# Kernel optimization log

Hardware: AMD Instinct MI355X
Metric: run time of the kernel (lower is better)

The kernel has to match this reference:

```python
import jax, jax.numpy as jnp
import numpy as np

B, C, H, W = 16, 256, 64, 64
D = C // 8  # query/key bottleneck dim


def setup_inputs() -> dict:
    key = jax.random.key(0)
    k1, k2, k3, k4 = jax.random.split(key, 4)
    x = jax.random.normal(k1, (B, C, H, W), dtype=jnp.float32)
    # 1x1 Conv1d weights (spectral-norm applied weights treated as given params)
    Wq = jax.random.normal(k2, (D, C), dtype=jnp.float32) * (1.0 / np.sqrt(C))
    Wk = jax.random.normal(k3, (D, C), dtype=jnp.float32) * (1.0 / np.sqrt(C))
    Wv = jax.random.normal(k4, (C, C), dtype=jnp.float32) * (1.0 / np.sqrt(C))
    gamma = jnp.array(0.5, dtype=jnp.float32)  # nonzero so attention path is exercised
    return {"x": x, "Wq": Wq, "Wk": Wk, "Wv": Wv, "gamma": gamma}


def reference(x, Wq, Wk, Wv, gamma):
    Bb, Cc, Hh, Ww = x.shape
    N = Hh * Ww
    flat = x.reshape(Bb, Cc, N)                    # [B, C, N]
    q = jnp.einsum('dc,bcn->bnd', Wq, flat)        # [B, N, D]
    k = jnp.einsum('dc,bcn->bdn', Wk, flat)        # [B, D, N]
    v = jnp.einsum('ec,bcn->ben', Wv, flat)        # [B, C, N]
    qk = jnp.einsum('bnd,bdm->bnm', q, k)          # [B, N, N]
    attn = jax.nn.softmax(qk, axis=1)              # NOTE: softmax over dim=1 (query axis), as in source
    out = jnp.einsum('ben,bnm->bem', v, attn)      # [B, C, N]
    out = out.reshape(Bb, Cc, Hh, Ww)
    return gamma * out + x
```

## Files before the change

### kernel.cpp

```cpp
#include <hip/hip_runtime.h>
#include <math.h>
#include <stdint.h>

#define NB 16
#define NC 256
#define NN 4096
#define ND 32

typedef __bf16 bf16_t;
typedef __bf16 bf16x4 __attribute__((ext_vector_type(4)));
typedef __bf16 bf16x8 __attribute__((ext_vector_type(8)));
typedef float  f32x4  __attribute__((ext_vector_type(4)));

#define AS_GLOBAL __attribute__((address_space(1)))
#define AS_LDS    __attribute__((address_space(3)))

__global__ __launch_bounds__(256) void wconv(
    const float* __restrict__ Wq, const float* __restrict__ Wk,
    const float* __restrict__ Wv, bf16_t* __restrict__ Wb, bf16_t* __restrict__ Wlo)
{
    int i = blockIdx.x * 256 + threadIdx.x;
    if (i >= 320 * 256) return;
    int row = i >> 8, c = i & 255;
    float v;
    if (row < 256)      v = Wv[(row      ) * 256 + c];
    else if (row < 288) v = Wq[(row - 256) * 256 + c] * 1.44269504088896340736f;
    else                v = Wk[(row - 288) * 256 + c];
    bf16_t h = (bf16_t)v;
    Wb[i] = h;
    if (row >= 256) Wlo[(row - 256) * 256 + c] = (bf16_t)(v - (float)h);
}

#define BN_P  128
#define KSTEP 64
#define XPAD  130

__global__ __launch_bounds__(512) void proj_mfma(
    const float* __restrict__ x, const bf16_t* __restrict__ Wb,
    const bf16_t* __restrict__ Wlo,
    bf16_t* __restrict__ Pqb, bf16_t* __restrict__ Pkb, bf16_t* __restrict__ Vn)
{
    __shared__ float xt[KSTEP][XPAD];

    const int b  = blockIdx.x >> 5;
    const int n0 = (blockIdx.x & 31) * BN_P;
    const int tid  = threadIdx.x;
    const int lane = tid & 63;
    const int w    = tid >> 6;
    const int mstrip = w >> 1;
    const int nh     = w & 1;
    const int llo = lane & 15, lhi = lane >> 4;
    const bool qkwave = (mstrip == 3);

    const float* xb = x + (size_t)b * NC * NN + n0;

    f32x4 acc[5][4];
    #pragma unroll
    for (int mf = 0; mf < 5; ++mf)
        #pragma unroll
        for (int nf = 0; nf < 4; ++nf)
            acc[mf][nf] = (f32x4){0.f,0.f,0.f,0.f};

    for (int k0 = 0; k0 < NC; k0 += KSTEP) {
        #pragma unroll
        for (int p = 0; p < 4; ++p) {
            int idx = p * 512 + tid;
            int c   = idx >> 5;
            int nn  = (idx & 31) << 2;
            float4 v = *(const float4*)(xb + (size_t)(k0 + c) * NN + nn);
            *(float2*)&xt[c][nn]     = make_float2(v.x, v.y);
            *(float2*)&xt[c][nn + 2] = make_float2(v.z, v.w);
        }
        __syncthreads();

        #pragma unroll
        for (int ks = 0; ks < 2; ++ks) {
            bf16x8 Ah[5], Al[4];
            #pragma unroll
            for (int mf = 0; mf < 5; ++mf) {
                int row = mstrip * 80 + mf * 16 + llo;
                Ah[mf] = *(const bf16x8*)(Wb + (size_t)row * NC + k0 + ks * 32 + lhi * 8);
            }
            if (qkwave) {
                #pragma unroll
                for (int mf = 1; mf < 5; ++mf) {
                    int row = mstrip * 80 + mf * 16 + llo;
                    Al[mf-1] = *(const bf16x8*)(Wlo + (size_t)(row - 256) * NC
                                                + k0 + ks * 32 + lhi * 8);
                }
            }

            #pragma unroll
            for (int nf = 0; nf < 4; ++nf) {
                const int n  = nh * 64 + nf * 16 + llo;
                const int cb = ks * 32 + lhi * 8;
                bf16x8 bh, bl;
                #pragma unroll
                for (int j = 0; j < 8; ++j) {
                    float f = xt[cb + j][n];
                    bf16_t h = (bf16_t)f;
                    bh[j] = h;
                    if (qkwave) bl[j] = (bf16_t)(f - (float)h);
                }
                #pragma unroll
                for (int mf = 0; mf < 5; ++mf)
                    acc[mf][nf] = __builtin_amdgcn_mfma_f32_16x16x32_bf16(
                                      Ah[mf], bh, acc[mf][nf], 0, 0, 0);
                if (qkwave) {
                    #pragma unroll
                    for (int mf = 1; mf < 5; ++mf) {
                        acc[mf][nf] = __builtin_amdgcn_mfma_f32_16x16x32_bf16(
                                          Al[mf-1], bh, acc[mf][nf], 0, 0, 0);
                        acc[mf][nf] = __builtin_amdgcn_mfma_f32_16x16x32_bf16(
                                          Ah[mf], bl, acc[mf][nf], 0, 0, 0);
                    }
                }
            }
        }
        __syncthreads();
    }

    #pragma unroll
    for (int mf = 0; mf < 5; ++mf) {
        const int rowbase = mstrip * 80 + mf * 16 + lhi * 4;
        #pragma unroll
        for (int nf = 0; nf < 4; ++nf) {
            const int n = n0 + nh * 64 + nf * 16 + llo;
            if (rowbase < 256) {
                #pragma unroll
                for (int r = 0; r < 4; ++r)
                    Vn[((size_t)b * NC + rowbase + r) * NN + n] = (bf16_t)acc[mf][nf][r];
            } else {
                const int d = rowbase - 256;
                bf16x4 q4;
                #pragma unroll
                for (int r = 0; r < 4; ++r) q4[r] = (bf16_t)acc[mf][nf][r];
                if (d < 32) *(bf16x4*)(Pqb + ((size_t)b * NN + n) * ND + d) = q4;
                else        *(bf16x4*)(Pkb + ((size_t)b * NN + n) * ND + d - 32) = q4;
            }
        }
    }
}

__global__ __launch_bounds__(512, 2) void attn_mfma(
    const bf16_t* __restrict__ Pqb,
    const bf16_t* __restrict__ Pkb,
    const bf16_t* __restrict__ Vn,
    const float* __restrict__ x,
    const float* __restrict__ gamma_p,
    float* __restrict__ y)
{
    __shared__ bf16_t vlds[2][256*64];
    __shared__ bf16_t plds[2][256*64];

    const int wg  = blockIdx.x;
    const int swb = (wg & 7) * 32 + (wg >> 3);
    const int b   = swb >> 4;
    const int m0  = (swb & 15) << 8;

    const int tid  = threadIdx.x;
    const int lane = tid & 63;
    const int w    = tid >> 6;
    const int lhi  = lane >> 4;
    const int llo  = lane & 15;
    const int wc   = w & 3;
    const int eh   = w >> 2;

    const bf16_t* Kbase = Pqb + (size_t)b * NN * ND;
    const bf16_t* Vball = Vn  + (size_t)b * NC * NN;

    bf16x8 qa[2];
    #pragma unroll
    for (int mq = 0; mq < 2; ++mq)
        qa[mq] = *(const bf16x8*)(Pkb + ((size_t)(b*NN + m0 + w*32 + mq*16 + llo)) * ND + lhi*8);

    f32x4 acc[8][4];
    #pragma unroll
    for (int et = 0; et < 8; ++et)
        #pragma unroll
        for (int mt = 0; mt < 4; ++mt)
            acc[et][mt] = (f32x4){0.f,0.f,0.f,0.f};

    float ps[2] = {0.f, 0.f};
    bf16x8 kb[4];
    const int swz = (llo & 7) << 4;

    const int r8  = lane >> 3;
    const int nsw = 8 * ((lane & 7) ^ r8);
    auto stageV = [&](int tt, int bufw) {
        #pragma unroll
        for (int i = 0; i < 4; ++i) {
            const int row0 = w*32 + i*8;
            const bf16_t* src = Vball + (size_t)(row0 + r8) * NN + tt*64 + nsw;
            bf16_t* dst = &vlds[bufw][row0 * 64];
            __builtin_amdgcn_global_load_lds(
                (const AS_GLOBAL unsigned int*)src,
                (AS_LDS unsigned int*)dst, 16, 0, 0);
        }
    };

    auto loadK = [&](int tt) {
        #pragma unroll
        for (int nt = 0; nt < 4; ++nt)
            kb[nt] = *(const bf16x8*)(Kbase + (size_t)(tt*64 + nt*16 + llo) * ND + lhi*8);
    };

    auto qk_phase = [&](int bufw) {
        f32x4 s[4][2];
        #pragma unroll
        for (int nt = 0; nt < 4; ++nt)
            #pragma unroll
            for (int mq = 0; mq < 2; ++mq)
                s[nt][mq] = __builtin_amdgcn_mfma_f32_16x16x32_bf16(kb[nt], qa[mq],
                                (f32x4){0.f,0.f,0.f,0.f}, 0, 0, 0);
        char* base = (char*)&plds[bufw][0] + (size_t)(w*32 + llo) * 128;
        #pragma unroll
        for (int mq = 0; mq < 2; ++mq)
            #pragma unroll
            for (int nt = 0; nt < 4; ++nt) {
                bf16x4 q4;
                #pragma unroll
                for (int r = 0; r < 4; ++r) {
                    float p = exp2f(s[nt][mq][r]);
                    ps[mq] += p;
                    q4[r] = (bf16_t)p;
                }
                *(bf16x4*)(base + mq*2048 + ((nt*32 + lhi*8) ^ swz)) = q4;
            }
    };

    auto pv_phase = [&](int bufw) {
        char* vb = (char*)&vlds[bufw][0];
        char* pb = (char*)&plds[bufw][0];
        #pragma unroll
        for (int ks = 0; ks < 2; ++ks) {
            const int cofs = (ks*64 + lhi*16) ^ swz;
            bf16x8 pf[4];
            #pragma unroll
            for (int mt = 0; mt < 4; ++mt) {
                const int row = wc*64 + mt*16 + llo;
                pf[mt] = *(const bf16x8*)(pb + (size_t)row*128 + cofs);
            }
            #pragma unroll
            for (int eg = 0; eg < 2; ++eg) {
                bf16x8 va[4];
                #pragma unroll
                for (int ei = 0; ei < 4; ++ei) {
                    const int row = eh*128 + (eg*4 + ei)*16 + llo;
                    va[ei] = *(const bf16x8*)(vb + (size_t)row*128 + cofs);
                }
                __builtin_amdgcn_s_setprio(1);
                #pragma unroll
                for (int ei = 0; ei < 4; ++ei)
                    #pragma unroll
                    for (int mt = 0; mt < 4; ++mt)
                        acc[eg*4 + ei][mt] = __builtin_amdgcn_mfma_f32_16x16x32_bf16(
                                          va[ei], pf[mt], acc[eg*4 + ei][mt], 0, 0, 0);
                __builtin_amdgcn_s_setprio(0);
            }
        }
    };

    stageV(0, 0);
    loadK(0);
    qk_phase(0);
    loadK(1);
    __syncthreads();

    for (int t = 0; t < NN/64; ++t) {
        const int cur = t & 1;
        const int nxt = cur ^ 1;
        if (t < NN/64 - 1) {
            stageV(t + 1, nxt);
            qk_phase(nxt);
        }
        if (t < NN/64 - 2) loadK(t + 2);
        pv_phase(cur);
        __syncthreads();
    }

    float* sum_lds = (float*)&vlds[0][0];
    #pragma unroll
    for (int mq = 0; mq < 2; ++mq) {
        float v = ps[mq];
        v += __shfl_xor(v, 16, 64);
        v += __shfl_xor(v, 32, 64);
        if (lhi == 0) sum_lds[w*32 + mq*16 + llo] = v;
    }
    __syncthreads();

    const float gamma = gamma_p[0];
    float inv[4];
    #pragma unroll
    for (int mt = 0; mt < 4; ++mt) inv[mt] = 1.f / sum_lds[wc*64 + mt*16 + llo];

    #pragma unroll
    for (int et = 0; et < 8; ++et)
        #pragma unroll
        for (int mt = 0; mt < 4; ++mt) {
            const int m = m0 + wc*64 + mt*16 + llo;
            #pragma unroll
            for (int r = 0; r < 4; ++r) {
                const int e = eh*128 + et*16 + lhi*4 + r;
                size_t idx = ((size_t)(b*NC + e)) * NN + m;
                y[idx] = gamma * (acc[et][mt][r] * inv[mt]) + x[idx];
            }
        }
}

extern "C" void kernel_launch(void* const* d_in, const int* in_sizes, int n_in,
                              void* d_out, int out_size, void* d_ws, size_t ws_size,
                              hipStream_t stream) {
    const float* x     = (const float*)d_in[0];
    const float* Wq    = (const float*)d_in[1];
    const float* Wk    = (const float*)d_in[2];
    const float* Wv    = (const float*)d_in[3];
    const float* gamma = (const float*)d_in[4];
    float* y = (float*)d_out;

    bf16_t* Pqb = (bf16_t*)d_ws;
    bf16_t* Pkb = Pqb + (size_t)NB * NN * ND;
    bf16_t* Vnb = Pkb + (size_t)NB * NN * ND;
    bf16_t* Wb  = Vnb + (size_t)NB * NC * NN;
    bf16_t* Wlo = Wb  + 320 * 256;

    wconv<<<320, 256, 0, stream>>>(Wq, Wk, Wv, Wb, Wlo);
    proj_mfma<<<NB * (NN / BN_P), 512, 0, stream>>>(x, Wb, Wlo, Pqb, Pkb, Vnb);
    attn_mfma<<<NB * (NN/256), 512, 0, stream>>>(Pqb, Pkb, Vnb, x, gamma, y);
}
```

Before: 225.5 us.

## Halve attention query tile to 128 and single-buffer V for higher occupancy

The attention kernel now handles 128 output columns per workgroup instead of 256. This halves the accumulator registers and P-tile LDS, and V is kept in a single LDS buffer, so launch bounds rise to 4 workgroups per CU. The loop adds a second barrier per iteration so the single V buffer can be refilled after the PV phase. The cost is that each V tile is loaded and reused by half as many query columns, which doubles global V traffic, and the extra barrier removes the V prefetch overlap. The raw exp2 builtin also replaces exp2f.

```diff
diff --git a/kernel.cpp b/kernel.cpp
--- a/kernel.cpp
+++ b/kernel.cpp
@@ -142,7 +142,7 @@
     }
 }
 
-__global__ __launch_bounds__(512, 2) void attn_mfma(
+__global__ __launch_bounds__(512, 4) void attn_mfma(
     const bf16_t* __restrict__ Pqb,
     const bf16_t* __restrict__ Pkb,
     const bf16_t* __restrict__ Vn,
@@ -150,13 +150,13 @@
     const float* __restrict__ gamma_p,
     float* __restrict__ y)
 {
-    __shared__ bf16_t vlds[2][256*64];
-    __shared__ bf16_t plds[2][256*64];
+    __shared__ bf16_t vlds[256*64];
+    __shared__ bf16_t plds[2][128*64];
 
     const int wg  = blockIdx.x;
-    const int swb = (wg & 7) * 32 + (wg >> 3);
-    const int b   = swb >> 4;
-    const int m0  = (swb & 15) << 8;
+    const int swb = (wg & 7) * 64 + (wg >> 3);
+    const int b   = swb >> 5;
+    const int m0  = (swb & 31) << 7;
 
     const int tid  = threadIdx.x;
     const int lane = tid & 63;
@@ -169,30 +169,27 @@
     const bf16_t* Kbase = Pqb + (size_t)b * NN * ND;
     const bf16_t* Vball = Vn  + (size_t)b * NC * NN;
 
-    bf16x8 qa[2];
-    #pragma unroll
-    for (int mq = 0; mq < 2; ++mq)
-        qa[mq] = *(const bf16x8*)(Pkb + ((size_t)(b*NN + m0 + w*32 + mq*16 + llo)) * ND + lhi*8);
-
-    f32x4 acc[8][4];
+    const bf16x8 qa = *(const bf16x8*)(Pkb + ((size_t)(b*NN + m0 + w*16 + llo)) * ND + lhi*8);
+
+    f32x4 acc[8][2];
     #pragma unroll
     for (int et = 0; et < 8; ++et)
         #pragma unroll
-        for (int mt = 0; mt < 4; ++mt)
+        for (int mt = 0; mt < 2; ++mt)
             acc[et][mt] = (f32x4){0.f,0.f,0.f,0.f};
 
-    float ps[2] = {0.f, 0.f};
+    float ps = 0.f;
     bf16x8 kb[4];
     const int swz = (llo & 7) << 4;
 
     const int r8  = lane >> 3;
     const int nsw = 8 * ((lane & 7) ^ r8);
-    auto stageV = [&](int tt, int bufw) {
+    auto stageV = [&](int tt) {
         #pragma unroll
         for (int i = 0; i < 4; ++i) {
             const int row0 = w*32 + i*8;
             const bf16_t* src = Vball + (size_t)(row0 + r8) * NN + tt*64 + nsw;
-            bf16_t* dst = &vlds[bufw][row0 * 64];
+            bf16_t* dst = &vlds[row0 * 64];
             __builtin_amdgcn_global_load_lds(
                 (const AS_GLOBAL unsigned int*)src,
                 (AS_LDS unsigned int*)dst, 16, 0, 0);
@@ -206,39 +203,35 @@
     };
 
     auto qk_phase = [&](int bufw) {
-        f32x4 s[4][2];
+        f32x4 s[4];
         #pragma unroll
         for (int nt = 0; nt < 4; ++nt)
-            #pragma unroll
-            for (int mq = 0; mq < 2; ++mq)
-                s[nt][mq] = __builtin_amdgcn_mfma_f32_16x16x32_bf16(kb[nt], qa[mq],
-                                (f32x4){0.f,0.f,0.f,0.f}, 0, 0, 0);
-        char* base = (char*)&plds[bufw][0] + (size_t)(w*32 + llo) * 128;
-        #pragma unroll
-        for (int mq = 0; mq < 2; ++mq)
-            #pragma unroll
-            for (int nt = 0; nt < 4; ++nt) {
-                bf16x4 q4;
-                #pragma unroll
-                for (int r = 0; r < 4; ++r) {
-                    float p = exp2f(s[nt][mq][r]);
-                    ps[mq] += p;
-                    q4[r] = (bf16_t)p;
-                }
-                *(bf16x4*)(base + mq*2048 + ((nt*32 + lhi*8) ^ swz)) = q4;
-            }
+            s[nt] = __builtin_amdgcn_mfma_f32_16x16x32_bf16(kb[nt], qa,
+                        (f32x4){0.f,0.f,0.f,0.f}, 0, 0, 0);
+        char* base = (char*)&plds[bufw][0] + (size_t)(w*16 + llo) * 128;
+        #pragma unroll
+        for (int nt = 0; nt < 4; ++nt) {
+            bf16x4 q4;
+            #pragma unroll
+            for (int r = 0; r < 4; ++r) {
+                float p = __builtin_amdgcn_exp2f(s[nt][r]);
+                ps += p;
+                q4[r] = (bf16_t)p;
+            }
+            *(bf16x4*)(base + ((nt*32 + lhi*8) ^ swz)) = q4;
+        }
     };
 
     auto pv_phase = [&](int bufw) {
-        char* vb = (char*)&vlds[bufw][0];
+        char* vb = (char*)&vlds[0];
         char* pb = (char*)&plds[bufw][0];
         #pragma unroll
         for (int ks = 0; ks < 2; ++ks) {
             const int cofs = (ks*64 + lhi*16) ^ swz;
-            bf16x8 pf[4];
-            #pragma unroll
-            for (int mt = 0; mt < 4; ++mt) {
-                const int row = wc*64 + mt*16 + llo;
+            bf16x8 pf[2];
+            #pragma unroll
+            for (int mt = 0; mt < 2; ++mt) {
+                const int row = wc*32 + mt*16 + llo;
                 pf[mt] = *(const bf16x8*)(pb + (size_t)row*128 + cofs);
             }
             #pragma unroll
@@ -253,7 +246,7 @@
                 #pragma unroll
                 for (int ei = 0; ei < 4; ++ei)
                     #pragma unroll
-                    for (int mt = 0; mt < 4; ++mt)
+                    for (int mt = 0; mt < 2; ++mt)
                         acc[eg*4 + ei][mt] = __builtin_amdgcn_mfma_f32_16x16x32_bf16(
                                           va[ei], pf[mt], acc[eg*4 + ei][mt], 0, 0, 0);
                 __builtin_amdgcn_s_setprio(0);
@@ -261,7 +254,7 @@
         }
     };
 
-    stageV(0, 0);
+    stageV(0);
     loadK(0);
     qk_phase(0);
     loadK(1);
@@ -269,36 +262,35 @@
 
     for (int t = 0; t < NN/64; ++t) {
         const int cur = t & 1;
-        const int nxt = cur ^ 1;
-        if (t < NN/64 - 1) {
-            stageV(t + 1, nxt);
-            qk_phase(nxt);
-        }
-        if (t < NN/64 - 2) loadK(t + 2);
         pv_phase(cur);
         __syncthreads();
+        if (t < NN/64 - 1) {
+            stageV(t + 1);
+            qk_phase(cur ^ 1);
+        }
+        if (t < NN/64 - 2) loadK(t + 2);
+        __syncthreads();
     }
 
-    float* sum_lds = (float*)&vlds[0][0];
-    #pragma unroll
-    for (int mq = 0; mq < 2; ++mq) {
-        float v = ps[mq];
+    float* sum_lds = (float*)&vlds[0];
+    {
+        float v = ps;
         v += __shfl_xor(v, 16, 64);
         v += __shfl_xor(v, 32, 64);
-        if (lhi == 0) sum_lds[w*32 + mq*16 + llo] = v;
+        if (lhi == 0) sum_lds[w*16 + llo] = v;
     }
     __syncthreads();
 
     const float gamma = gamma_p[0];
-    float inv[4];
-    #pragma unroll
-    for (int mt = 0; mt < 4; ++mt) inv[mt] = 1.f / sum_lds[wc*64 + mt*16 + llo];
+    float inv[2];
+    #pragma unroll
+    for (int mt = 0; mt < 2; ++mt) inv[mt] = 1.f / sum_lds[wc*32 + mt*16 + llo];
 
     #pragma unroll
     for (int et = 0; et < 8; ++et)
         #pragma unroll
-        for (int mt = 0; mt < 4; ++mt) {
-            const int m = m0 + wc*64 + mt*16 + llo;
+        for (int mt = 0; mt < 2; ++mt) {
+            const int m = m0 + wc*32 + mt*16 + llo;
             #pragma unroll
             for (int r = 0; r < 4; ++r) {
                 const int e = eh*128 + et*16 + lhi*4 + r;
@@ -326,5 +318,5 @@
 
     wconv<<<320, 256, 0, stream>>>(Wq, Wk, Wv, Wb, Wlo);
     proj_mfma<<<NB * (NN / BN_P), 512, 0, stream>>>(x, Wb, Wlo, Pqb, Pkb, Vnb);
-    attn_mfma<<<NB * (NN/256), 512, 0, stream>>>(Pqb, Pkb, Vnb, x, gamma, y);
+    attn_mfma<<<NB * (NN/128), 512, 0, stream>>>(Pqb, Pkb, Vnb, x, gamma, y);
 }
```

Result: slower. 236.0 us (+4.7%).

## Unroll attention loop by two with ping-pong K registers and explicit waitcnt barriers

Applied to the files above, without the earlier changes.

The main N-loop is unrolled by two, with two K register sets swapped in turn so the next-next K tile loads while the current tiles are computed. The `__syncthreads` at the end of each iteration becomes a partial `s_waitcnt vmcnt(4)` plus `s_barrier` at the start. This lets the K prefetch stay in flight across the barrier while the staged V tile is still guaranteed complete. The PV phase now loads all eight V fragments before its MFMA burst, and `exp2f` becomes the raw hardware exp2 builtin. The risks are higher register pressure and correctness that depends on the hand-counted vmcnt.

```diff
diff --git a/kernel.cpp b/kernel.cpp
--- a/kernel.cpp
+++ b/kernel.cpp
@@ -182,7 +182,7 @@
             acc[et][mt] = (f32x4){0.f,0.f,0.f,0.f};
 
     float ps[2] = {0.f, 0.f};
-    bf16x8 kb[4];
+    bf16x8 kbA[4], kbB[4];
     const int swz = (llo & 7) << 4;
 
     const int r8  = lane >> 3;
@@ -199,13 +199,13 @@
         }
     };
 
-    auto loadK = [&](int tt) {
+    auto loadKinto = [&](int tt, bf16x8* kb) {
         #pragma unroll
         for (int nt = 0; nt < 4; ++nt)
             kb[nt] = *(const bf16x8*)(Kbase + (size_t)(tt*64 + nt*16 + llo) * ND + lhi*8);
     };
 
-    auto qk_phase = [&](int bufw) {
+    auto qk_phase = [&](const bf16x8* kb, int bufw) {
         f32x4 s[4][2];
         #pragma unroll
         for (int nt = 0; nt < 4; ++nt)
@@ -221,7 +221,7 @@
                 bf16x4 q4;
                 #pragma unroll
                 for (int r = 0; r < 4; ++r) {
-                    float p = exp2f(s[nt][mq][r]);
+                    float p = __builtin_amdgcn_exp2f(s[nt][mq][r]);
                     ps[mq] += p;
                     q4[r] = (bf16_t)p;
                 }
@@ -241,43 +241,50 @@
                 const int row = wc*64 + mt*16 + llo;
                 pf[mt] = *(const bf16x8*)(pb + (size_t)row*128 + cofs);
             }
-            #pragma unroll
-            for (int eg = 0; eg < 2; ++eg) {
-                bf16x8 va[4];
-                #pragma unroll
-                for (int ei = 0; ei < 4; ++ei) {
-                    const int row = eh*128 + (eg*4 + ei)*16 + llo;
-                    va[ei] = *(const bf16x8*)(vb + (size_t)row*128 + cofs);
-                }
-                __builtin_amdgcn_s_setprio(1);
-                #pragma unroll
-                for (int ei = 0; ei < 4; ++ei)
-                    #pragma unroll
-                    for (int mt = 0; mt < 4; ++mt)
-                        acc[eg*4 + ei][mt] = __builtin_amdgcn_mfma_f32_16x16x32_bf16(
-                                          va[ei], pf[mt], acc[eg*4 + ei][mt], 0, 0, 0);
-                __builtin_amdgcn_s_setprio(0);
-            }
+            bf16x8 va[8];
+            #pragma unroll
+            for (int ei = 0; ei < 8; ++ei) {
+                const int row = eh*128 + ei*16 + llo;
+                va[ei] = *(const bf16x8*)(vb + (size_t)row*128 + cofs);
+            }
+            __builtin_amdgcn_s_setprio(1);
+            #pragma unroll
+            for (int ei = 0; ei < 8; ++ei)
+                #pragma unroll
+                for (int mt = 0; mt < 4; ++mt)
+                    acc[ei][mt] = __builtin_amdgcn_mfma_f32_16x16x32_bf16(
+                                      va[ei], pf[mt], acc[ei][mt], 0, 0, 0);
+            __builtin_amdgcn_s_setprio(0);
         }
     };
 
+    loadKinto(0, kbA);
     stageV(0, 0);
-    loadK(0);
-    qk_phase(0);
-    loadK(1);
+    loadKinto(1, kbB);
+    qk_phase(kbA, 0);
+
+    for (int t = 0; t < NN/64; t += 2) {
+        if (t + 2 < NN/64) loadKinto(t + 2, kbA);
+        if (t < NN/64 - 2) asm volatile("s_waitcnt vmcnt(4)" ::: "memory");
+        else               asm volatile("s_waitcnt vmcnt(0)" ::: "memory");
+        asm volatile("s_waitcnt lgkmcnt(0)" ::: "memory");
+        __builtin_amdgcn_s_barrier();
+        __builtin_amdgcn_sched_barrier(0);
+        if (t + 1 < NN/64) { stageV(t + 1, 1); qk_phase(kbB, 1); }
+        pv_phase(0);
+
+        const int u = t + 1;
+        if (u + 2 < NN/64) loadKinto(u + 2, kbB);
+        if (u < NN/64 - 2) asm volatile("s_waitcnt vmcnt(4)" ::: "memory");
+        else               asm volatile("s_waitcnt vmcnt(0)" ::: "memory");
+        asm volatile("s_waitcnt lgkmcnt(0)" ::: "memory");
+        __builtin_amdgcn_s_barrier();
+        __builtin_amdgcn_sched_barrier(0);
+        if (u + 1 < NN/64) { stageV(u + 1, 0); qk_phase(kbA, 0); }
+        pv_phase(1);
+    }
+
     __syncthreads();
-
-    for (int t = 0; t < NN/64; ++t) {
-        const int cur = t & 1;
-        const int nxt = cur ^ 1;
-        if (t < NN/64 - 1) {
-            stageV(t + 1, nxt);
-            qk_phase(nxt);
-        }
-        if (t < NN/64 - 2) loadK(t + 2);
-        pv_phase(cur);
-        __syncthreads();
-    }
 
     float* sum_lds = (float*)&vlds[0][0];
     #pragma unroll
```

After: 521.1 us. +131.1%, slower.
